# Performance work log

Measured on AMD Instinct MI355X. Metric: run time of the kernel, lower is better.

## Reference

```python
import jax, jax.numpy as jnp
import numpy as np


def setup_inputs() -> dict:
    key = jax.random.key(0)
    kx, ka, kb, kc, kw, ke = jax.random.split(key, 6)
    B, T = 4096, 8192
    x = jax.random.normal(kx, (B, T), dtype=jnp.float32)
    a = jax.random.uniform(ka, (1,), jnp.float32, 0.95, 0.999)
    b = jax.random.uniform(kb, (1,), jnp.float32, -0.5, 0.5)
    c = jax.random.uniform(kc, (1,), jnp.float32, -0.1, 0.1)
    w = jax.random.uniform(kw, (1,), jnp.float32, -0.5, 0.5)
    e = jax.random.uniform(ke, (1,), jnp.float32, -0.1, 0.1)
    return {"x": x, "a": a, "b": b, "c": c, "w": w, "e": e}


def reference(x, a, b, c, w, e):
    # x: [B, T]; a,b,c,w,e: [1] scalar params.
    # Linear recurrence h_t = a*h_{t-1} + b*x_t + c, h_{-1}=0; output z = w*h_T + e.
    h0 = jnp.zeros((x.shape[0],), dtype=x.dtype)  # [B]

    def step(h, xt):
        return a * h + b * xt + c, None

    hT, _ = jax.lax.scan(step, h0, x.T)  # scan over T, carry [B]
    return w * hT + e  # [B]
```

## Files before the change

### kernel.cpp

```cpp
#include <hip/hip_runtime.h>


constexpr int T_LEN = 8192;
constexpr int BLOCK = 256;
constexpr int CHUNKS = T_LEN / (BLOCK * 4);

__global__ __launch_bounds__(BLOCK) void recur_row_kernel(
    const float* __restrict__ x,
    const float* __restrict__ pa, const float* __restrict__ pb,
    const float* __restrict__ pc, const float* __restrict__ pw,
    const float* __restrict__ pe, float* __restrict__ out)
{
    const int row = blockIdx.x;
    const int j = threadIdx.x;

    const float a = pa[0];
    const float b = pb[0];
    const float c = pc[0];
    const float w = pw[0];
    const float e = pe[0];

    const double ad = (double)a;
    double a1024d = ad;
    #pragma unroll
    for (int i = 0; i < 10; ++i) a1024d *= a1024d;
    const float A1024 = (float)a1024d;

    int expn = 4 * (BLOCK - 1 - j);
    double wgt_d = 1.0, base = ad;
    while (expn) { if (expn & 1) wgt_d *= base; base *= base; expn >>= 1; }
    const float wgt = (float)wgt_d;

    const float4* xr = reinterpret_cast<const float4*>(x + (size_t)row * T_LEN);
    float p = 0.0f;
    #pragma unroll
    for (int u = 0; u < CHUNKS; ++u) {
        float4 v = xr[u * BLOCK + j];
        float q = ((v.x * a + v.y) * a + v.z) * a + v.w;
        p = A1024 * p + q;
    }
    float part = wgt * p;

    #pragma unroll
    for (int off = 32; off > 0; off >>= 1)
        part += __shfl_down(part, off, 64);

    __shared__ float sred[BLOCK / 64];
    const int lane = j & 63, wid = j >> 6;
    if (lane == 0) sred[wid] = part;
    __syncthreads();

    if (j == 0) {
        float D = sred[0] + sred[1] + sred[2] + sred[3];
        double a8192 = a1024d * a1024d;
        a8192 *= a8192;
        a8192 *= a8192;
        double S = (1.0 - a8192) / (1.0 - ad);
        out[row] = w * (b * D + c * (float)S) + e;
    }
}

extern "C" void kernel_launch(void* const* d_in, const int* in_sizes, int n_in,
                              void* d_out, int out_size, void* d_ws, size_t ws_size,
                              hipStream_t stream) {
    const float* x  = (const float*)d_in[0];
    const float* pa = (const float*)d_in[1];
    const float* pb = (const float*)d_in[2];
    const float* pc = (const float*)d_in[3];
    const float* pw = (const float*)d_in[4];
    const float* pe = (const float*)d_in[5];
    float* out = (float*)d_out;

    const int B = out_size;
    recur_row_kernel<<<dim3(B), dim3(BLOCK), 0, stream>>>(x, pa, pb, pc, pw, pe, out);
}
```

Measured before the change: 25.68 us.

## Map one wavefront per row and use nontemporal vector loads

Each 64-lane wavefront now reduces a whole row, so a 256-thread block covers four rows. This removes the shared-memory reduction and the block barrier. Each lane handles 32 float4 chunks, combined with a^256 scaling. Loads use nontemporal hints to avoid polluting the cache. The trade-off is longer per-thread dependency chains and four times fewer blocks.

```diff
diff --git a/kernel.cpp b/kernel.cpp
--- a/kernel.cpp
+++ b/kernel.cpp
@@ -3,7 +3,10 @@
 
 constexpr int T_LEN = 8192;
 constexpr int BLOCK = 256;
-constexpr int CHUNKS = T_LEN / (BLOCK * 4);
+constexpr int ROWS_PER_BLOCK = BLOCK / 64;
+constexpr int CHUNKS = T_LEN / (64 * 4);
+
+typedef float vfloat4 __attribute__((ext_vector_type(4)));
 
 __global__ __launch_bounds__(BLOCK) void recur_row_kernel(
     const float* __restrict__ x,
@@ -11,8 +14,9 @@
     const float* __restrict__ pc, const float* __restrict__ pw,
     const float* __restrict__ pe, float* __restrict__ out)
 {
-    const int row = blockIdx.x;
-    const int j = threadIdx.x;
+    const int wid  = threadIdx.x >> 6;
+    const int lane = threadIdx.x & 63;
+    const int row  = blockIdx.x * ROWS_PER_BLOCK + wid;
 
     const float a = pa[0];
     const float b = pb[0];
@@ -21,23 +25,23 @@
     const float e = pe[0];
 
     const double ad = (double)a;
-    double a1024d = ad;
+    double a256d = ad;
     #pragma unroll
-    for (int i = 0; i < 10; ++i) a1024d *= a1024d;
-    const float A1024 = (float)a1024d;
+    for (int i = 0; i < 8; ++i) a256d *= a256d;
+    const float A256 = (float)a256d;
 
-    int expn = 4 * (BLOCK - 1 - j);
+    int expn = 4 * (63 - lane);
     double wgt_d = 1.0, base = ad;
     while (expn) { if (expn & 1) wgt_d *= base; base *= base; expn >>= 1; }
     const float wgt = (float)wgt_d;
 
-    const float4* xr = reinterpret_cast<const float4*>(x + (size_t)row * T_LEN);
+    const vfloat4* xr = reinterpret_cast<const vfloat4*>(x + (size_t)row * T_LEN);
     float p = 0.0f;
     #pragma unroll
     for (int u = 0; u < CHUNKS; ++u) {
-        float4 v = xr[u * BLOCK + j];
+        vfloat4 v = __builtin_nontemporal_load(&xr[u * 64 + lane]);
         float q = ((v.x * a + v.y) * a + v.z) * a + v.w;
-        p = A1024 * p + q;
+        p = A256 * p + q;
     }
     float part = wgt * p;
 
@@ -45,18 +49,14 @@
     for (int off = 32; off > 0; off >>= 1)
         part += __shfl_down(part, off, 64);
 
-    __shared__ float sred[BLOCK / 64];
-    const int lane = j & 63, wid = j >> 6;
-    if (lane == 0) sred[wid] = part;
-    __syncthreads();
-
-    if (j == 0) {
-        float D = sred[0] + sred[1] + sred[2] + sred[3];
-        double a8192 = a1024d * a1024d;
+    if (lane == 0) {
+        double a8192 = a256d * a256d;
+        a8192 *= a8192;
+        a8192 *= a8192;
         a8192 *= a8192;
         a8192 *= a8192;
         double S = (1.0 - a8192) / (1.0 - ad);
-        out[row] = w * (b * D + c * (float)S) + e;
+        out[row] = w * (b * part + c * (float)S) + e;
     }
 }
 
@@ -72,5 +72,6 @@
     float* out = (float*)d_out;
 
     const int B = out_size;
-    recur_row_kernel<<<dim3(B), dim3(BLOCK), 0, stream>>>(x, pa, pb, pc, pw, pe, out);
+    recur_row_kernel<<<dim3(B / ROWS_PER_BLOCK), dim3(BLOCK), 0, stream>>>(
+        x, pa, pb, pc, pw, pe, out);
 }
```

Result: faster. 24.49 us (-4.6%).
